# Kernel tuning notes

Measured on AMD Instinct MI355X. Metric: run time of the kernel, lower is better.

Reference implementation:

```python
import jax, jax.numpy as jnp
import numpy as np

EMB = 1024
HEADS = 16
BLOCK = 128


def setup_inputs() -> dict:
    key = jax.random.key(0)
    k1, k2, k3 = jax.random.split(key, 3)
    B, T, C = 4, 4096, EMB
    x = jax.random.normal(k1, (B, T, C), dtype=jnp.float32)
    # Linear weights stored as [in, out] (i.e. torch W.T); qkv has no bias.
    W_qkv = jax.random.normal(k2, (C, 3 * C), dtype=jnp.float32) * 0.02
    W_proj = jax.random.normal(k3, (C, C), dtype=jnp.float32) * 0.02
    b_proj = jnp.zeros((C,), dtype=jnp.float32)
    return {"x": x, "W_qkv": W_qkv, "W_proj": W_proj, "b_proj": b_proj}


def reference(x, W_qkv, W_proj, b_proj):
    # Dropout is inference-mode identity.
    B, T, C = x.shape
    H, D, BS = HEADS, C // HEADS, BLOCK
    nb = T // BS  # number of local blocks
    qkv = x @ W_qkv  # [B,T,3C]
    q, k, v = jnp.split(qkv, 3, axis=-1)
    # [B, nb, BS, H, D] -- each block attends only within itself
    q = q.reshape(B, nb, BS, H, D)
    k = k.reshape(B, nb, BS, H, D)
    v = v.reshape(B, nb, BS, H, D)
    scores = jnp.einsum("bnqhd,bnkhd->bnhqk", q, k) / jnp.sqrt(jnp.float32(D))
    # is_decoder: causal tril within each diagonal block (tril[i:end, i:end])
    tril = jnp.tril(jnp.ones((BS, BS), dtype=bool))
    scores = jnp.where(tril, scores, -jnp.inf)
    # faithful to original: stable exp, then divide by (sum + 1e-6)
    scores = scores - jnp.max(scores, axis=-1, keepdims=True)
    e = jnp.exp(scores)
    p = e / (jnp.sum(e, axis=-1, keepdims=True) + 1e-6)
    out = jnp.einsum("bnhqk,bnkhd->bnqhd", p, v).reshape(B, T, C)
    return out @ W_proj + b_proj
```

## Files before the change

kernel.cpp:

```cpp
#include <hip/hip_runtime.h>
#include <hip/hip_bf16.h>
#include <math.h>


typedef __bf16 bf16_t;
typedef __bf16 bf16x8 __attribute__((ext_vector_type(8)));
typedef float  f32x4  __attribute__((ext_vector_type(4)));

typedef const __attribute__((address_space(1))) void* gptr_t;
typedef __attribute__((address_space(3))) void* lptr_t;

__global__ __launch_bounds__(256) void prepass(const float* __restrict__ x,
                                               bf16_t* __restrict__ xb,
                                               const float* __restrict__ Wqkv,
                                               bf16_t* __restrict__ wqkvT,
                                               const float* __restrict__ Wproj,
                                               bf16_t* __restrict__ wprojT) {
    __shared__ float tile[32][33];
    const int bid = blockIdx.x;
    if (bid < 8192) {
        const size_t n = (size_t)16384 * 1024;
        const size_t stride = (size_t)8192 * 256 * 4;
        for (size_t i = ((size_t)bid * 256 + threadIdx.x) * 4; i < n; i += stride) {
            float4 v = *(const float4*)(x + i);
            bf16_t t[4];
            t[0] = (bf16_t)v.x; t[1] = (bf16_t)v.y; t[2] = (bf16_t)v.z; t[3] = (bf16_t)v.w;
            *(uint2*)(xb + i) = *(uint2*)t;
        }
        return;
    }
    const float* in;
    bf16_t* out;
    int K, N, bx, by;
    if (bid < 8192 + 3072) {
        const int t = bid - 8192;
        in = Wqkv; out = wqkvT; K = 1024; N = 3072;
        bx = t % 96; by = t / 96;
    } else {
        const int t = bid - 11264;
        in = Wproj; out = wprojT; K = 1024; N = 1024;
        bx = t & 31; by = t >> 5;
    }
    const int tx = threadIdx.x & 31, ty = threadIdx.x >> 5;
    #pragma unroll
    for (int i = 0; i < 4; i++) {
        const int k = by * 32 + ty + i * 8;
        tile[ty + i * 8][tx] = in[(size_t)k * N + bx * 32 + tx];
    }
    __syncthreads();
    #pragma unroll
    for (int i = 0; i < 4; i++) {
        const int n = bx * 32 + ty + i * 8;
        out[(size_t)n * K + by * 32 + tx] = (bf16_t)tile[tx][ty + i * 8];
    }
}

template <bool BF16_OUT, bool BIAS>
__global__ __launch_bounds__(256, 2) void gemm256x128(const bf16_t* __restrict__ A,
                                                      const bf16_t* __restrict__ Bt,
                                                      void* __restrict__ Cout,
                                                      const float* __restrict__ bias,
                                                      int M, int N, int K) {
    __shared__ bf16_t ring[3][12288];

    const int tid  = threadIdx.x;
    const int lane = tid & 63, wave = tid >> 6;
    const int quad = lane >> 4, l16 = lane & 15;
    const int wm = wave >> 1, wn = wave & 1;

    const int nbm  = M >> 8;
    const int mloc = nbm >> 3;
    const int xcd  = blockIdx.x & 7;
    const int idx  = blockIdx.x >> 3;
    const int bn   = idx / mloc;
    const int bm   = xcd * mloc + (idx - bn * mloc);

    const bf16_t* Ab = A  + (size_t)bm * 256 * K;
    const bf16_t* Bb = Bt + (size_t)bn * 128 * K;

    const int srow = lane >> 2;
    const int scs  = (lane & 3) ^ ((srow >> 1) & 3);
    const int rdo  = ((quad ^ ((l16 >> 1) & 3)) << 3);

    f32x4 acc[8][4];
    #pragma unroll
    for (int i = 0; i < 8; ++i)
        #pragma unroll
        for (int j = 0; j < 4; ++j) acc[i][j] = (f32x4){0.f, 0.f, 0.f, 0.f};

#define STG(SLICE, SLOT)                                                              \
    do {                                                                              \
        _Pragma("unroll")                                                             \
        for (int i_ = 0; i_ < 4; ++i_)                                                \
            __builtin_amdgcn_global_load_lds(                                         \
                (gptr_t)(Ab + (size_t)(wave * 64 + i_ * 16 + srow) * K +              \
                         ((SLICE) << 5) + scs * 8),                                   \
                (lptr_t)&ring[SLOT][(wave * 64 + i_ * 16) * 32], 16, 0, 0);           \
        _Pragma("unroll")                                                             \
        for (int i_ = 0; i_ < 2; ++i_)                                                \
            __builtin_amdgcn_global_load_lds(                                         \
                (gptr_t)(Bb + (size_t)(wave * 32 + i_ * 16 + srow) * K +              \
                         ((SLICE) << 5) + scs * 8),                                   \
                (lptr_t)&ring[SLOT][8192 + (wave * 32 + i_ * 16) * 32], 16, 0, 0);    \
    } while (0)

#define BODY(G, RS, SS, DO_STAGE, WAIT_STMT)                                          \
    do {                                                                              \
        const bf16_t* sl_ = ring[RS];                                                 \
        bf16x8 af_[8], bf_[4];                                                        \
        _Pragma("unroll")                                                             \
        for (int fr = 0; fr < 8; ++fr)                                                \
            af_[fr] = *(const bf16x8*)&sl_[(wm * 128 + fr * 16 + l16) * 32 + rdo];    \
        _Pragma("unroll")                                                             \
        for (int fr = 0; fr < 4; ++fr)                                                \
            bf_[fr] =                                                                 \
                *(const bf16x8*)&sl_[8192 + (wn * 64 + fr * 16 + l16) * 32 + rdo];    \
        if (DO_STAGE) STG((G) + 2, SS);                                               \
        asm volatile("s_waitcnt lgkmcnt(0)" ::: "memory");                            \
        WAIT_STMT;                                                                    \
        __builtin_amdgcn_s_barrier();                                                 \
        __builtin_amdgcn_s_setprio(1);                                                \
        _Pragma("unroll")                                                             \
        for (int mr = 0; mr < 8; ++mr)                                                \
            _Pragma("unroll")                                                         \
            for (int nr = 0; nr < 4; ++nr)                                            \
                acc[mr][nr] = __builtin_amdgcn_mfma_f32_16x16x32_bf16(                \
                    af_[mr], bf_[nr], acc[mr][nr], 0, 0, 0);                          \
        __builtin_amdgcn_s_setprio(0);                                                \
    } while (0)

    STG(0, 0); STG(1, 1);
    asm volatile("s_waitcnt vmcnt(6)" ::: "memory");
    __builtin_amdgcn_s_barrier();

    const int NS = K >> 5;
    int rs = 0, ss = 2;
    for (int g = 0; g < NS - 2; ++g) {
        BODY(g, rs, ss, true, asm volatile("s_waitcnt vmcnt(6)" ::: "memory"));
        rs = (rs == 2) ? 0 : rs + 1;
        ss = (ss == 2) ? 0 : ss + 1;
    }
    BODY(NS - 2, rs, ss, false, asm volatile("s_waitcnt vmcnt(0)" ::: "memory"));
    rs = (rs == 2) ? 0 : rs + 1;
    BODY(NS - 1, rs, ss, false, (void)0);
#undef BODY
#undef STG

    #pragma unroll
    for (int mr = 0; mr < 8; ++mr) {
        #pragma unroll
        for (int nr = 0; nr < 4; ++nr) {
            const int gcol = bn * 128 + wn * 64 + nr * 16 + l16;
            #pragma unroll
            for (int reg = 0; reg < 4; ++reg) {
                const int grow = bm * 256 + wm * 128 + mr * 16 + quad * 4 + reg;
                float v = acc[mr][nr][reg];
                if (BIAS) v += bias[gcol];
                if (BF16_OUT)
                    ((bf16_t*)Cout)[(size_t)grow * N + gcol] = (bf16_t)v;
                else
                    ((float*)Cout)[(size_t)grow * N + gcol] = v;
            }
        }
    }
}

__global__ __launch_bounds__(256, 3) void attn_kernel(const bf16_t* __restrict__ qkv,
                                                      bf16_t* __restrict__ attn_out) {
    __shared__ __align__(16) char smem[54272];
    bf16_t* qs = (bf16_t*)smem;
    bf16_t* ks = (bf16_t*)(smem + 18432);
    bf16_t* vT = (bf16_t*)(smem + 36864);
    bf16_t* ps = (bf16_t*)smem;

    const int tid = threadIdx.x;
    const int lane = tid & 63, wave = tid >> 6;
    const int quad = lane >> 4, l16 = lane & 15;

    const int bid = blockIdx.x;
    const int h = bid & 15;
    const int blk = (bid >> 4) & 31;
    const int b = bid >> 9;
    const int row0 = (b * 32 + blk) * 128;
    const int LDQ = 3072;

    for (int t = tid; t < 128 * 8; t += 256) {
        const int r = t >> 3;
        const int c = (t & 7) * 8;
        const bf16_t* src = qkv + (size_t)(row0 + r) * LDQ + h * 64;
        *(uint4*)&qs[r * 72 + c] = *(const uint4*)(src + c);
        *(uint4*)&ks[r * 72 + c] = *(const uint4*)(src + 1024 + c);
        bf16x8 vv = *(const bf16x8*)(src + 2048 + c);
        #pragma unroll
        for (int j = 0; j < 8; j++)
            vT[(c + j) * 136 + r] = vv[j];
    }
    __syncthreads();

    f32x4 sfrag[2][8];
    for (int mr = 0; mr < 2; mr++)
        for (int nc = 0; nc < 8; nc++)
            sfrag[mr][nc] = (f32x4){0.f, 0.f, 0.f, 0.f};

    #pragma unroll
    for (int ksl = 0; ksl < 2; ksl++) {
        bf16x8 aq[2], bk[8];
        #pragma unroll
        for (int mr = 0; mr < 2; mr++)
            aq[mr] = *(const bf16x8*)&qs[(wave * 32 + mr * 16 + l16) * 72 + ksl * 32 + quad * 8];
        #pragma unroll
        for (int nc = 0; nc < 8; nc++)
            bk[nc] = *(const bf16x8*)&ks[(nc * 16 + l16) * 72 + ksl * 32 + quad * 8];
        #pragma unroll
        for (int mr = 0; mr < 2; mr++)
            #pragma unroll
            for (int nc = 0; nc < 8; nc++)
                sfrag[mr][nc] = __builtin_amdgcn_mfma_f32_16x16x32_bf16(aq[mr], bk[nc], sfrag[mr][nc], 0, 0, 0);
    }

    #pragma unroll
    for (int mr = 0; mr < 2; mr++) {
        #pragma unroll
        for (int nc = 0; nc < 8; nc++) {
            #pragma unroll
            for (int reg = 0; reg < 4; reg++) {
                const int row = wave * 32 + mr * 16 + quad * 4 + reg;
                const int col = nc * 16 + l16;
                float s = sfrag[mr][nc][reg] * 0.125f;
                if (col > row) s = -INFINITY;
                sfrag[mr][nc][reg] = s;
            }
        }
    }

    #pragma unroll
    for (int mr = 0; mr < 2; mr++) {
        #pragma unroll
        for (int reg = 0; reg < 4; reg++) {
            float m = -INFINITY;
            #pragma unroll
            for (int nc = 0; nc < 8; nc++) m = fmaxf(m, sfrag[mr][nc][reg]);
            #pragma unroll
            for (int off = 1; off < 16; off <<= 1) m = fmaxf(m, __shfl_xor(m, off));
            float sum = 0.f;
            #pragma unroll
            for (int nc = 0; nc < 8; nc++) {
                float e = __expf(sfrag[mr][nc][reg] - m);
                sfrag[mr][nc][reg] = e;
                sum += e;
            }
            #pragma unroll
            for (int off = 1; off < 16; off <<= 1) sum += __shfl_xor(sum, off);
            const float inv = 1.0f / (sum + 1e-6f);
            #pragma unroll
            for (int nc = 0; nc < 8; nc++) sfrag[mr][nc][reg] *= inv;
        }
    }

    __syncthreads();

    #pragma unroll
    for (int mr = 0; mr < 2; mr++)
        #pragma unroll
        for (int nc = 0; nc < 8; nc++)
            #pragma unroll
            for (int reg = 0; reg < 4; reg++) {
                const int row = wave * 32 + mr * 16 + quad * 4 + reg;
                const int col = nc * 16 + l16;
                ps[row * 136 + col] = (bf16_t)sfrag[mr][nc][reg];
            }
    __syncthreads();

    f32x4 oacc[2][4];
    for (int mr = 0; mr < 2; mr++)
        for (int nd = 0; nd < 4; nd++)
            oacc[mr][nd] = (f32x4){0.f, 0.f, 0.f, 0.f};

    #pragma unroll
    for (int ksl = 0; ksl < 4; ksl++) {
        bf16x8 ap[2];
        #pragma unroll
        for (int mr = 0; mr < 2; mr++)
            ap[mr] = *(const bf16x8*)&ps[(wave * 32 + mr * 16 + l16) * 136 + ksl * 32 + quad * 8];
        #pragma unroll
        for (int nd = 0; nd < 4; nd++) {
            bf16x8 bv = *(const bf16x8*)&vT[(nd * 16 + l16) * 136 + ksl * 32 + quad * 8];
            #pragma unroll
            for (int mr = 0; mr < 2; mr++)
                oacc[mr][nd] = __builtin_amdgcn_mfma_f32_16x16x32_bf16(ap[mr], bv, oacc[mr][nd], 0, 0, 0);
        }
    }

    #pragma unroll
    for (int mr = 0; mr < 2; mr++)
        #pragma unroll
        for (int nd = 0; nd < 4; nd++)
            #pragma unroll
            for (int reg = 0; reg < 4; reg++) {
                const int row = row0 + wave * 32 + mr * 16 + quad * 4 + reg;
                const int col = h * 64 + nd * 16 + l16;
                attn_out[(size_t)row * 1024 + col] = (bf16_t)oacc[mr][nd][reg];
            }
}

extern "C" void kernel_launch(void* const* d_in, const int* in_sizes, int n_in,
                              void* d_out, int out_size, void* d_ws, size_t ws_size,
                              hipStream_t stream) {
    const float* x     = (const float*)d_in[0];
    const float* Wqkv  = (const float*)d_in[1];
    const float* Wproj = (const float*)d_in[2];
    const float* bproj = (const float*)d_in[3];

    const int M = 16384, C = 1024, N1 = 3072;

    char* ws = (char*)d_ws;
    bf16_t* xb     = (bf16_t*)(ws);
    bf16_t* wqkvT  = (bf16_t*)(ws + 33554432);
    bf16_t* wprojT = (bf16_t*)(ws + 39845888);
    bf16_t* qkvb   = (bf16_t*)(ws + 41943040);
    bf16_t* attnb  = (bf16_t*)(ws + 142606336);

    prepass<<<12288, 256, 0, stream>>>(x, xb, Wqkv, wqkvT, Wproj, wprojT);

    gemm256x128<true, false><<<(N1 / 128) * (M / 256), 256, 0, stream>>>(
        xb, wqkvT, (void*)qkvb, nullptr, M, N1, C);

    attn_kernel<<<2048, 256, 0, stream>>>(qkvb, attnb);

    gemm256x128<false, true><<<(C / 128) * (M / 256), 256, 0, stream>>>(
        attnb, wprojT, d_out, bproj, M, C, C);
}
```

Before: 315.2 us.

## Retile GEMMs to 256x256 with 16 waves and swizzle attention V transpose

Both projection GEMMs move from 256x128 tiles with 4 waves to 256x256 tiles with 1024-thread blocks. Each wave now computes a 64x64 sub-tile, and the explicit lgkmcnt wait is dropped. This raises operand reuse per staged tile and halves the grid, but the larger LDS ring and the launch bound of 4 blocks may cut registers and occupancy. The attention kernel also gets an XCD-aware block-to-head mapping and a paired-row, XOR-swizzled V transpose, to reduce LDS bank conflicts and scattered 16-bit stores.

```diff
diff --git a/kernel.cpp b/kernel.cpp
--- a/kernel.cpp
+++ b/kernel.cpp
@@ -5,6 +5,7 @@
 
 typedef __bf16 bf16_t;
 typedef __bf16 bf16x8 __attribute__((ext_vector_type(8)));
+typedef unsigned short u16x8 __attribute__((ext_vector_type(8)));
 typedef float  f32x4  __attribute__((ext_vector_type(4)));
 
 typedef const __attribute__((address_space(1))) void* gptr_t;
@@ -56,17 +57,17 @@
 }
 
 template <bool BF16_OUT, bool BIAS>
-__global__ __launch_bounds__(256, 2) void gemm256x128(const bf16_t* __restrict__ A,
-                                                      const bf16_t* __restrict__ Bt,
-                                                      void* __restrict__ Cout,
-                                                      const float* __restrict__ bias,
-                                                      int M, int N, int K) {
-    __shared__ bf16_t ring[3][12288];
+__global__ __launch_bounds__(1024, 4) void gemm256q(const bf16_t* __restrict__ A,
+                                                    const bf16_t* __restrict__ Bt,
+                                                    void* __restrict__ Cout,
+                                                    const float* __restrict__ bias,
+                                                    int M, int N, int K) {
+    __shared__ bf16_t ring[3][16384];
 
     const int tid  = threadIdx.x;
     const int lane = tid & 63, wave = tid >> 6;
     const int quad = lane >> 4, l16 = lane & 15;
-    const int wm = wave >> 1, wn = wave & 1;
+    const int wm = wave >> 2, wn = wave & 3;
 
     const int nbm  = M >> 8;
     const int mloc = nbm >> 3;
@@ -76,52 +77,45 @@
     const int bm   = xcd * mloc + (idx - bn * mloc);
 
     const bf16_t* Ab = A  + (size_t)bm * 256 * K;
-    const bf16_t* Bb = Bt + (size_t)bn * 128 * K;
+    const bf16_t* Bb = Bt + (size_t)bn * 256 * K;
 
     const int srow = lane >> 2;
     const int scs  = (lane & 3) ^ ((srow >> 1) & 3);
     const int rdo  = ((quad ^ ((l16 >> 1) & 3)) << 3);
 
-    f32x4 acc[8][4];
-    #pragma unroll
-    for (int i = 0; i < 8; ++i)
+    f32x4 acc[4][4];
+    #pragma unroll
+    for (int i = 0; i < 4; ++i)
         #pragma unroll
         for (int j = 0; j < 4; ++j) acc[i][j] = (f32x4){0.f, 0.f, 0.f, 0.f};
 
 #define STG(SLICE, SLOT)                                                              \
     do {                                                                              \
-        _Pragma("unroll")                                                             \
-        for (int i_ = 0; i_ < 4; ++i_)                                                \
-            __builtin_amdgcn_global_load_lds(                                         \
-                (gptr_t)(Ab + (size_t)(wave * 64 + i_ * 16 + srow) * K +              \
-                         ((SLICE) << 5) + scs * 8),                                   \
-                (lptr_t)&ring[SLOT][(wave * 64 + i_ * 16) * 32], 16, 0, 0);           \
-        _Pragma("unroll")                                                             \
-        for (int i_ = 0; i_ < 2; ++i_)                                                \
-            __builtin_amdgcn_global_load_lds(                                         \
-                (gptr_t)(Bb + (size_t)(wave * 32 + i_ * 16 + srow) * K +              \
-                         ((SLICE) << 5) + scs * 8),                                   \
-                (lptr_t)&ring[SLOT][8192 + (wave * 32 + i_ * 16) * 32], 16, 0, 0);    \
+        __builtin_amdgcn_global_load_lds(                                             \
+            (gptr_t)(Ab + (size_t)(wave * 16 + srow) * K + ((SLICE) << 5) + scs * 8), \
+            (lptr_t)&ring[SLOT][wave * 512], 16, 0, 0);                               \
+        __builtin_amdgcn_global_load_lds(                                             \
+            (gptr_t)(Bb + (size_t)(wave * 16 + srow) * K + ((SLICE) << 5) + scs * 8), \
+            (lptr_t)&ring[SLOT][8192 + wave * 512], 16, 0, 0);                        \
     } while (0)
 
 #define BODY(G, RS, SS, DO_STAGE, WAIT_STMT)                                          \
     do {                                                                              \
         const bf16_t* sl_ = ring[RS];                                                 \
-        bf16x8 af_[8], bf_[4];                                                        \
+        bf16x8 af_[4], bf_[4];                                                        \
         _Pragma("unroll")                                                             \
-        for (int fr = 0; fr < 8; ++fr)                                                \
-            af_[fr] = *(const bf16x8*)&sl_[(wm * 128 + fr * 16 + l16) * 32 + rdo];    \
+        for (int fr = 0; fr < 4; ++fr)                                                \
+            af_[fr] = *(const bf16x8*)&sl_[(wm * 64 + fr * 16 + l16) * 32 + rdo];     \
         _Pragma("unroll")                                                             \
         for (int fr = 0; fr < 4; ++fr)                                                \
             bf_[fr] =                                                                 \
                 *(const bf16x8*)&sl_[8192 + (wn * 64 + fr * 16 + l16) * 32 + rdo];    \
         if (DO_STAGE) STG((G) + 2, SS);                                               \
-        asm volatile("s_waitcnt lgkmcnt(0)" ::: "memory");                            \
         WAIT_STMT;                                                                    \
         __builtin_amdgcn_s_barrier();                                                 \
         __builtin_amdgcn_s_setprio(1);                                                \
         _Pragma("unroll")                                                             \
-        for (int mr = 0; mr < 8; ++mr)                                                \
+        for (int mr = 0; mr < 4; ++mr)                                                \
             _Pragma("unroll")                                                         \
             for (int nr = 0; nr < 4; ++nr)                                            \
                 acc[mr][nr] = __builtin_amdgcn_mfma_f32_16x16x32_bf16(                \
@@ -130,13 +124,13 @@
     } while (0)
 
     STG(0, 0); STG(1, 1);
-    asm volatile("s_waitcnt vmcnt(6)" ::: "memory");
+    asm volatile("s_waitcnt vmcnt(2)" ::: "memory");
     __builtin_amdgcn_s_barrier();
 
     const int NS = K >> 5;
     int rs = 0, ss = 2;
     for (int g = 0; g < NS - 2; ++g) {
-        BODY(g, rs, ss, true, asm volatile("s_waitcnt vmcnt(6)" ::: "memory"));
+        BODY(g, rs, ss, true, asm volatile("s_waitcnt vmcnt(2)" ::: "memory"));
         rs = (rs == 2) ? 0 : rs + 1;
         ss = (ss == 2) ? 0 : ss + 1;
     }
@@ -147,13 +141,13 @@
 #undef STG
 
     #pragma unroll
-    for (int mr = 0; mr < 8; ++mr) {
+    for (int mr = 0; mr < 4; ++mr) {
         #pragma unroll
         for (int nr = 0; nr < 4; ++nr) {
-            const int gcol = bn * 128 + wn * 64 + nr * 16 + l16;
+            const int gcol = bn * 256 + wn * 64 + nr * 16 + l16;
             #pragma unroll
             for (int reg = 0; reg < 4; ++reg) {
-                const int grow = bm * 256 + wm * 128 + mr * 16 + quad * 4 + reg;
+                const int grow = bm * 256 + wm * 64 + mr * 16 + quad * 4 + reg;
                 float v = acc[mr][nr][reg];
                 if (BIAS) v += bias[gcol];
                 if (BF16_OUT)
@@ -177,10 +171,13 @@
     const int lane = tid & 63, wave = tid >> 6;
     const int quad = lane >> 4, l16 = lane & 15;
 
-    const int bid = blockIdx.x;
-    const int h = bid & 15;
-    const int blk = (bid >> 4) & 31;
-    const int b = bid >> 9;
+    const int gid = blockIdx.x;
+    const int xcd = gid & 7;
+    const int j = gid >> 3;
+    const int h = j & 15;
+    const int blkhi = (j >> 4) & 3;
+    const int b = j >> 6;
+    const int blk = blkhi * 8 + xcd;
     const int row0 = (b * 32 + blk) * 128;
     const int LDQ = 3072;
 
@@ -190,10 +187,19 @@
         const bf16_t* src = qkv + (size_t)(row0 + r) * LDQ + h * 64;
         *(uint4*)&qs[r * 72 + c] = *(const uint4*)(src + c);
         *(uint4*)&ks[r * 72 + c] = *(const uint4*)(src + 1024 + c);
-        bf16x8 vv = *(const bf16x8*)(src + 2048 + c);
-        #pragma unroll
-        for (int j = 0; j < 8; j++)
-            vT[(c + j) * 136 + r] = vv[j];
+    }
+    for (int t = tid; t < 64 * 8; t += 256) {
+        const int r2 = t >> 3;
+        const int c0 = (t & 7) * 8;
+        const bf16_t* vsrc = qkv + (size_t)(row0 + 2 * r2) * LDQ + h * 64 + 2048 + c0;
+        u16x8 v0 = *(const u16x8*)(vsrc);
+        u16x8 v1 = *(const u16x8*)(vsrc + LDQ);
+        const int X = (t & 7) << 3;
+        #pragma unroll
+        for (int jj = 0; jj < 8; jj++) {
+            unsigned int pv = (unsigned int)v0[jj] | ((unsigned int)v1[jj] << 16);
+            *(unsigned int*)&vT[(c0 + jj) * 136 + ((2 * r2) ^ X)] = pv;
+        }
     }
     __syncthreads();
 
@@ -284,7 +290,9 @@
             ap[mr] = *(const bf16x8*)&ps[(wave * 32 + mr * 16 + l16) * 136 + ksl * 32 + quad * 8];
         #pragma unroll
         for (int nd = 0; nd < 4; nd++) {
-            bf16x8 bv = *(const bf16x8*)&vT[(nd * 16 + l16) * 136 + ksl * 32 + quad * 8];
+            const int c2 = nd * 16 + l16;
+            const int X2 = ((c2 >> 3) & 7) << 3;
+            bf16x8 bv = *(const bf16x8*)&vT[c2 * 136 + ((ksl * 32 + quad * 8) ^ X2)];
             #pragma unroll
             for (int mr = 0; mr < 2; mr++)
                 oacc[mr][nd] = __builtin_amdgcn_mfma_f32_16x16x32_bf16(ap[mr], bv, oacc[mr][nd], 0, 0, 0);
@@ -322,11 +330,11 @@
 
     prepass<<<12288, 256, 0, stream>>>(x, xb, Wqkv, wqkvT, Wproj, wprojT);
 
-    gemm256x128<true, false><<<(N1 / 128) * (M / 256), 256, 0, stream>>>(
+    gemm256q<true, false><<<(N1 / 256) * (M / 256), 1024, 0, stream>>>(
         xb, wqkvT, (void*)qkvb, nullptr, M, N1, C);
 
     attn_kernel<<<2048, 256, 0, stream>>>(qkvb, attnb);
 
-    gemm256x128<false, true><<<(C / 128) * (M / 256), 256, 0, stream>>>(
+    gemm256q<false, true><<<(C / 256) * (M / 256), 1024, 0, stream>>>(
         attnb, wprojT, d_out, bproj, M, C, C);
 }
```

Result: faster. 300.9 us (-4.5%).
